# Kernel optimization log

Hardware: AMD Instinct MI355X
Metric: run time of the kernel (lower is better)

## Reference

```python
import jax, jax.numpy as jnp
import numpy as np


def setup_inputs() -> dict:
    key = jax.random.key(0)
    k1, k2 = jax.random.split(key)
    B, N, M, D = 4, 8192, 8192, 3
    pred = jax.random.normal(k1, (B, N, D), dtype=jnp.float32)
    target = jax.random.normal(k2, (B, M, D), dtype=jnp.float32)
    return {"pred": pred, "target": target}


def reference(pred, target):
    # Pairwise squared distances via the GEMM cross-term trick:
    # ||p - t||^2 = ||p||^2 + ||t||^2 - 2 <p, t>
    pn = jnp.sum(pred * pred, axis=-1)            # [B, N]
    tn = jnp.sum(target * target, axis=-1)        # [B, M]
    cross = jnp.einsum('bnd,bmd->bnm', pred, target)  # [B, N, M]
    dist = pn[:, :, None] + tn[:, None, :] - 2.0 * cross
    d_pt = jnp.min(dist, axis=2)  # [B, N] pred -> nearest target
    d_tp = jnp.min(dist, axis=1)  # [B, M] target -> nearest pred
    return jnp.mean(d_pt) + jnp.mean(d_tp)
```

## Files before the change

kernel.cpp:

```cpp
#include <hip/hip_runtime.h>
#include <hip/hip_bf16.h>


typedef __attribute__((ext_vector_type(8)))  short short8;
typedef __attribute__((ext_vector_type(16))) float f32x16;

#define BATCH 4
#define NPTS 8192
#define TOTALQ (BATCH * NPTS)
#define BLK 256
#define WNT 4
#define BCOLS 512
#define MSPLIT 8
#define MC (NPTS / MSPLIT)
#define MT_PER (MC / 32)

__device__ __forceinline__ unsigned short f2bf(float f) {
    unsigned int u = __float_as_uint(f);
    u += 0x7FFFu + ((u >> 16) & 1u);
    return (unsigned short)(u >> 16);
}
__device__ __forceinline__ float bf2f(unsigned short h) {
    return __uint_as_float(((unsigned int)h) << 16);
}
__device__ __forceinline__ unsigned int pk2(unsigned short a, unsigned short b) {
    return (unsigned int)a | ((unsigned int)b << 16);
}

struct Payload {
    unsigned short hx, hy, hz, lx, ly, lz, n1, n2, n3;
};
__device__ __forceinline__ Payload split_point(float x, float y, float z) {
    Payload P;
    P.hx = f2bf(x);  P.hy = f2bf(y);  P.hz = f2bf(z);
    P.lx = f2bf(x - bf2f(P.hx));
    P.ly = f2bf(y - bf2f(P.hy));
    P.lz = f2bf(z - bf2f(P.hz));
    float nrm = fmaf(z, z, fmaf(y, y, x * x));
    P.n1 = f2bf(nrm);
    float r1 = nrm - bf2f(P.n1);
    P.n2 = f2bf(r1);
    P.n3 = f2bf(r1 - bf2f(P.n2));
    return P;
}

__global__ __launch_bounds__(BLK) void chamfer_mega_kernel(
        const float* __restrict__ pred, const float* __restrict__ target,
        float* __restrict__ part, float* __restrict__ out)
{
    const int dir = blockIdx.z;
    const float* __restrict__ Q  = dir ? target : pred;
    const float* __restrict__ Tg = dir ? pred : target;

    const int nch = blockIdx.x;
    const int b   = nch >> 4;
    const int ms  = blockIdx.y;
    const int w    = threadIdx.x >> 6;
    const int lane = threadIdx.x & 63;
    const int c = lane & 31;
    const int g = lane >> 5;
    const unsigned short ONE = 0x3F80;

    if (blockIdx.x == 0 && blockIdx.y == 0 && blockIdx.z == 0 &&
        threadIdx.x == 0) out[0] = 0.0f;

    __shared__ uint4 ldsb[2][MC];

    #pragma unroll
    for (int j = 0; j < MC / BLK; ++j) {
        int p = j * BLK + threadIdx.x;
        size_t gp = (size_t)b * NPTS + (size_t)ms * MC + p;
        float x = Tg[3 * gp], y = Tg[3 * gp + 1], z = Tg[3 * gp + 2];
        Payload P = split_point(x, y, z);
        ldsb[0][p] = (uint4){ pk2(P.hx, P.hy), pk2(P.hz, P.hx),
                              pk2(P.hy, P.hz), pk2(P.lx, P.ly) };
        ldsb[1][p] = (uint4){ pk2(P.lz, ONE), pk2(ONE, ONE),
                              pk2(P.n1, P.n2), pk2(P.n3, 0) };
    }

    const int colstart = nch * BCOLS + w * (WNT * 32);
    short8 bq[WNT];
    #pragma unroll
    for (int nt = 0; nt < WNT; ++nt) {
        int r = colstart + nt * 32 + c;
        float x = Q[3 * r], y = Q[3 * r + 1], z = Q[3 * r + 2];
        Payload P = split_point(x, y, z);
        unsigned short ax = f2bf(-2.f * bf2f(P.hx)),
                       ay = f2bf(-2.f * bf2f(P.hy)),
                       az = f2bf(-2.f * bf2f(P.hz));
        unsigned short cx = f2bf(-2.f * bf2f(P.lx)),
                       cy = f2bf(-2.f * bf2f(P.ly)),
                       cz = f2bf(-2.f * bf2f(P.lz));
        uint4 h0 = { pk2(ax, ay), pk2(az, cx), pk2(cy, cz), pk2(ax, ay) };
        uint4 h1 = { pk2(az, P.n1), pk2(P.n2, P.n3), pk2(ONE, ONE), pk2(ONE, 0) };
        uint4 sel = g ? h1 : h0;
        bq[nt] = *(short8*)&sel;
    }

    f32x16 acc[WNT];
    #pragma unroll
    for (int nt = 0; nt < WNT; ++nt)
        #pragma unroll
        for (int r = 0; r < 16; ++r) acc[nt][r] = 3.4e38f;

    f32x16 vzero;
    #pragma unroll
    for (int r = 0; r < 16; ++r) vzero[r] = 0.0f;

    __syncthreads();

    const ushort* ldsu = (const ushort*)&ldsb[g][0];

    for (int mt = 0; mt < MT_PER; mt += 2) {
        short8 at0 = *(const short8*)(ldsu + (mt * 32 + c) * 8);
        short8 at1 = *(const short8*)(ldsu + ((mt + 1) * 32 + c) * 8);
        #pragma unroll
        for (int nt = 0; nt < WNT; ++nt) {
            f32x16 d0, d1;
            asm("v_mfma_f32_32x32x16_bf16 %0, %2, %4, %5\n\t"
                "v_mfma_f32_32x32x16_bf16 %1, %3, %4, %5\n\t"
                "s_nop 7\n\t"
                "s_nop 7"
                : "=&v"(d0), "=&v"(d1)
                : "v"(at0), "v"(at1), "v"(bq[nt]), "v"(vzero));
            #pragma unroll
            for (int r = 0; r < 16; ++r)
                acc[nt][r] = fminf(fminf(acc[nt][r], d0[r]), d1[r]);
        }
    }

    float* rp = part + (size_t)(dir * MSPLIT + ms) * TOTALQ;
    #pragma unroll
    for (int nt = 0; nt < WNT; ++nt) {
        f32x16 v = acc[nt];
        float m0 = fminf(fminf(v[0],  v[1]),  fminf(v[2],  v[3]));
        float m1 = fminf(fminf(v[4],  v[5]),  fminf(v[6],  v[7]));
        float m2 = fminf(fminf(v[8],  v[9]),  fminf(v[10], v[11]));
        float m3 = fminf(fminf(v[12], v[13]), fminf(v[14], v[15]));
        float m  = fminf(fminf(m0, m1), fminf(m2, m3));
        m = fminf(m, __shfl_xor(m, 32, 64));
        if (g == 0) rp[colstart + nt * 32 + c] = m;
    }
}

__global__ __launch_bounds__(BLK) void chamfer_reduce_kernel(
        const float* __restrict__ part, float* __restrict__ out)
{
    int gl = blockIdx.x * BLK + threadIdx.x;
    int dir = gl >> 15, i = gl & (TOTALQ - 1);

    const float* p = part + (size_t)dir * MSPLIT * TOTALQ + i;
    float m = p[0];
    #pragma unroll
    for (int s = 1; s < MSPLIT; ++s)
        m = fminf(m, p[(size_t)s * TOTALQ]);

    float acc = m * (1.0f / (float)TOTALQ);
    #pragma unroll
    for (int off = 32; off > 0; off >>= 1)
        acc += __shfl_down(acc, off, 64);
    __shared__ float wsum[BLK / 64];
    int lane = threadIdx.x & 63, wid = threadIdx.x >> 6;
    if (lane == 0) wsum[wid] = acc;
    __syncthreads();
    if (threadIdx.x == 0) {
        float s = 0.0f;
        #pragma unroll
        for (int wv = 0; wv < BLK / 64; ++wv) s += wsum[wv];
        atomicAdd(out, s);
    }
}

extern "C" void kernel_launch(void* const* d_in, const int* in_sizes, int n_in,
                              void* d_out, int out_size, void* d_ws, size_t ws_size,
                              hipStream_t stream) {
    const float* pred   = (const float*)d_in[0];
    const float* target = (const float*)d_in[1];
    float*       out    = (float*)d_out;
    float*       part   = (float*)d_ws;

    dim3 grid(TOTALQ / BCOLS, MSPLIT, 2);
    hipLaunchKernelGGL(chamfer_mega_kernel, grid, dim3(BLK), 0, stream,
                       pred, target, part, out);

    hipLaunchKernelGGL(chamfer_reduce_kernel, dim3(2 * TOTALQ / BLK), dim3(BLK),
                       0, stream, (const float*)part, out);
}
```

Before: 76.82 us.

## Precompute bf16 split payloads in a prep kernel and stream A tiles from global

Adds a prep kernel that converts every pred and target point once into packed bf16 hi/lo/norm payloads for both MFMA operand roles and stores them in workspace. The main kernel then loads B fragments and A tiles straight from global memory instead of recomputing the split per block and staging it through LDS, dropping the LDS buffer and the barrier. WNT is halved so the grid has twice as many blocks. This removes redundant conversion work and LDS occupancy limits, but adds a launch, extra global traffic, and global-load latency inside the MFMA loop.

```diff
diff --git a/kernel.cpp b/kernel.cpp
--- a/kernel.cpp
+++ b/kernel.cpp
@@ -1,5 +1,4 @@
 #include <hip/hip_runtime.h>
-#include <hip/hip_bf16.h>
 
 
 typedef __attribute__((ext_vector_type(8)))  short short8;
@@ -9,11 +8,18 @@
 #define NPTS 8192
 #define TOTALQ (BATCH * NPTS)
 #define BLK 256
-#define WNT 4
-#define BCOLS 512
+#define WNT 2
+#define BCOLS (4 * WNT * 32)
+#define NCHUNK (TOTALQ / BCOLS)
 #define MSPLIT 8
 #define MC (NPTS / MSPLIT)
 #define MT_PER (MC / 32)
+
+#define PAY_APRED 0
+#define PAY_ATARG (2 * TOTALQ)
+#define PAY_BPRED (4 * TOTALQ)
+#define PAY_BTARG (6 * TOTALQ)
+#define PART_OFF_BYTES ((size_t)(8 * TOTALQ) * 16)
 
 __device__ __forceinline__ unsigned short f2bf(float f) {
     unsigned int u = __float_as_uint(f);
@@ -44,57 +50,59 @@
     return P;
 }
 
+__global__ __launch_bounds__(BLK) void chamfer_prep_kernel(
+        const float* __restrict__ pred, const float* __restrict__ target,
+        uint4* __restrict__ pay, float* __restrict__ out)
+{
+    int t = blockIdx.x * BLK + threadIdx.x;
+    if (t == 0) out[0] = 0.0f;
+    int which = t >> 15;
+    int i = t & (TOTALQ - 1);
+    const float* __restrict__ src = which ? target : pred;
+    float x = src[3 * i], y = src[3 * i + 1], z = src[3 * i + 2];
+    Payload P = split_point(x, y, z);
+    const unsigned short ONE = 0x3F80;
+
+    int abase = (which ? PAY_ATARG : PAY_APRED) + 2 * i;
+    pay[abase]     = (uint4){ pk2(P.hx, P.hy), pk2(P.hz, P.hx),
+                              pk2(P.hy, P.hz), pk2(P.lx, P.ly) };
+    pay[abase + 1] = (uint4){ pk2(P.lz, ONE), pk2(ONE, ONE),
+                              pk2(P.n1, P.n2), pk2(P.n3, 0) };
+
+    unsigned short ax = f2bf(-2.f * bf2f(P.hx)),
+                   ay = f2bf(-2.f * bf2f(P.hy)),
+                   az = f2bf(-2.f * bf2f(P.hz));
+    unsigned short cx = f2bf(-2.f * bf2f(P.lx)),
+                   cy = f2bf(-2.f * bf2f(P.ly)),
+                   cz = f2bf(-2.f * bf2f(P.lz));
+    int bbase = (which ? PAY_BTARG : PAY_BPRED) + 2 * i;
+    pay[bbase]     = (uint4){ pk2(ax, ay), pk2(az, cx), pk2(cy, cz), pk2(ax, ay) };
+    pay[bbase + 1] = (uint4){ pk2(az, P.n1), pk2(P.n2, P.n3),
+                              pk2(ONE, ONE), pk2(ONE, 0) };
+}
+
 __global__ __launch_bounds__(BLK) void chamfer_mega_kernel(
-        const float* __restrict__ pred, const float* __restrict__ target,
-        float* __restrict__ part, float* __restrict__ out)
+        const uint4* __restrict__ pay, float* __restrict__ part)
 {
     const int dir = blockIdx.z;
-    const float* __restrict__ Q  = dir ? target : pred;
-    const float* __restrict__ Tg = dir ? pred : target;
-
     const int nch = blockIdx.x;
-    const int b   = nch >> 4;
+    const int b   = nch >> 5;
     const int ms  = blockIdx.y;
     const int w    = threadIdx.x >> 6;
     const int lane = threadIdx.x & 63;
     const int c = lane & 31;
     const int g = lane >> 5;
-    const unsigned short ONE = 0x3F80;
 
-    if (blockIdx.x == 0 && blockIdx.y == 0 && blockIdx.z == 0 &&
-        threadIdx.x == 0) out[0] = 0.0f;
-
-    __shared__ uint4 ldsb[2][MC];
-
-    #pragma unroll
-    for (int j = 0; j < MC / BLK; ++j) {
-        int p = j * BLK + threadIdx.x;
-        size_t gp = (size_t)b * NPTS + (size_t)ms * MC + p;
-        float x = Tg[3 * gp], y = Tg[3 * gp + 1], z = Tg[3 * gp + 2];
-        Payload P = split_point(x, y, z);
-        ldsb[0][p] = (uint4){ pk2(P.hx, P.hy), pk2(P.hz, P.hx),
-                              pk2(P.hy, P.hz), pk2(P.lx, P.ly) };
-        ldsb[1][p] = (uint4){ pk2(P.lz, ONE), pk2(ONE, ONE),
-                              pk2(P.n1, P.n2), pk2(P.n3, 0) };
-    }
+    const uint4* __restrict__ Ap = pay + (dir ? PAY_APRED : PAY_ATARG)
+                                 + (size_t)(b * NPTS + ms * MC) * 2;
+    const uint4* __restrict__ Bq = pay + (dir ? PAY_BTARG : PAY_BPRED);
 
     const int colstart = nch * BCOLS + w * (WNT * 32);
     short8 bq[WNT];
     #pragma unroll
     for (int nt = 0; nt < WNT; ++nt) {
-        int r = colstart + nt * 32 + c;
-        float x = Q[3 * r], y = Q[3 * r + 1], z = Q[3 * r + 2];
-        Payload P = split_point(x, y, z);
-        unsigned short ax = f2bf(-2.f * bf2f(P.hx)),
-                       ay = f2bf(-2.f * bf2f(P.hy)),
-                       az = f2bf(-2.f * bf2f(P.hz));
-        unsigned short cx = f2bf(-2.f * bf2f(P.lx)),
-                       cy = f2bf(-2.f * bf2f(P.ly)),
-                       cz = f2bf(-2.f * bf2f(P.lz));
-        uint4 h0 = { pk2(ax, ay), pk2(az, cx), pk2(cy, cz), pk2(ax, ay) };
-        uint4 h1 = { pk2(az, P.n1), pk2(P.n2, P.n3), pk2(ONE, ONE), pk2(ONE, 0) };
-        uint4 sel = g ? h1 : h0;
-        bq[nt] = *(short8*)&sel;
+        uint4 v = Bq[2 * (colstart + nt * 32 + c) + g];
+        bq[nt] = *(short8*)&v;
     }
 
     f32x16 acc[WNT];
@@ -107,13 +115,12 @@
     #pragma unroll
     for (int r = 0; r < 16; ++r) vzero[r] = 0.0f;
 
-    __syncthreads();
-
-    const ushort* ldsu = (const ushort*)&ldsb[g][0];
-
+    #pragma unroll 4
     for (int mt = 0; mt < MT_PER; mt += 2) {
-        short8 at0 = *(const short8*)(ldsu + (mt * 32 + c) * 8);
-        short8 at1 = *(const short8*)(ldsu + ((mt + 1) * 32 + c) * 8);
+        uint4 va0 = Ap[(mt * 32 + c) * 2 + g];
+        uint4 va1 = Ap[((mt + 1) * 32 + c) * 2 + g];
+        short8 at0 = *(short8*)&va0;
+        short8 at1 = *(short8*)&va1;
         #pragma unroll
         for (int nt = 0; nt < WNT; ++nt) {
             f32x16 d0, d1;
@@ -177,11 +184,15 @@
     const float* pred   = (const float*)d_in[0];
     const float* target = (const float*)d_in[1];
     float*       out    = (float*)d_out;
-    float*       part   = (float*)d_ws;
+    uint4*       pay    = (uint4*)d_ws;
+    float*       part   = (float*)((char*)d_ws + PART_OFF_BYTES);
 
-    dim3 grid(TOTALQ / BCOLS, MSPLIT, 2);
+    hipLaunchKernelGGL(chamfer_prep_kernel, dim3(2 * TOTALQ / BLK), dim3(BLK),
+                       0, stream, pred, target, pay, out);
+
+    dim3 grid(NCHUNK, MSPLIT, 2);
     hipLaunchKernelGGL(chamfer_mega_kernel, grid, dim3(BLK), 0, stream,
-                       pred, target, part, out);
+                       pay, part);
 
     hipLaunchKernelGGL(chamfer_reduce_kernel, dim3(2 * TOTALQ / BLK), dim3(BLK),
                        0, stream, (const float*)part, out);
```

Result: slower. 80.53 us (+4.8%).
